# Kernel optimization log

Hardware: AMD Instinct MI355X
Metric: run time of the kernel (lower is better)

Reference implementation:

```python
import jax, jax.numpy as jnp
import numpy as np

N_NODES = 10000
N_EDGES = 320000
F_NODE = 16
NUM_BESSEL = 8
M = 32           # env_embed_multiplicity
LAT = 128        # latent dimension
R_MAX = 5.0
P_CUT = 6.0      # polynomial cutoff order
AVG_NEIGH = 32.0
SQRT3 = 1.7320508075688772
SQRT2 = 1.4142135623730951


def _mlp(x, weights):
    # nequip ScalarMLPFunction: linear layers with 1/sqrt(fan_in) norm, silu between layers
    h = x
    n = len(weights)
    for i, W in enumerate(weights):
        h = h @ W * (1.0 / np.sqrt(W.shape[0]))
        if i < n - 1:
            h = jax.nn.silu(h)
    return h


def _weight_channels(Y, w):
    # MakeWeightedChannels: Y [E,4] = (0e | 1e), w [E,M,2] per-irrep weights -> [E,M,4]
    return jnp.concatenate([w[..., 0:1] * Y[:, None, 0:1],
                            w[..., 1:2] * Y[:, None, 1:4]], axis=-1)


def setup_inputs():
    key = jax.random.key(0)
    ks = jax.random.split(key, 16)

    def w(k, i, o):
        return jax.random.normal(k, (i, o), jnp.float32)

    two_body_in = 2 * F_NODE + NUM_BESSEL  # 40
    return {
        "coordinates": jax.random.uniform(ks[0], (N_NODES, 3), jnp.float32),
        "node_attrs": jax.random.uniform(ks[1], (N_NODES, F_NODE), jnp.float32),
        "edge_index": jax.random.randint(ks[2], (2, N_EDGES), 0, N_NODES),
        "W2b0": w(ks[3], two_body_in, 64),
        "W2b1": w(ks[4], 64, 128),
        "W2b2": w(ks[5], 128, LAT),
        "Wenv0": w(ks[6], LAT, 4 * M),       # initial-edge embed + env weights (2 irreps each)
        "Wlat0": w(ks[7], LAT + 2 * M, 128),
        "Wlat1": w(ks[8], 128, LAT),
        "Ws0": w(ks[9], 2 * M, M),            # e3nn Linear, scalar block (2 paths)
        "Wv0": w(ks[10], 3 * M, M),           # e3nn Linear, vector block (3 paths)
        "Wenv1": w(ks[11], LAT, 2 * M),
        "Wfin0": w(ks[12], LAT + 2 * M, 128),
        "Wfin1": w(ks[13], 128, LAT),
    }


def reference(coordinates, node_attrs, edge_index, W2b0, W2b1, W2b2, Wenv0,
              Wlat0, Wlat1, Ws0, Wv0, Wenv1, Wfin0, Wfin1):
    sender, center = edge_index[0], edge_index[1]
    vec = coordinates[center] - coordinates[sender]            # [E,3]
    r = jnp.sqrt(jnp.sum(vec * vec, axis=-1) + 1e-12)          # [E]
    u = r / R_MAX
    p = P_CUT
    fcut = (1.0 - (p + 1.0) * (p + 2.0) / 2.0 * u**p
            + p * (p + 2.0) * u**(p + 1.0)
            - p * (p + 1.0) / 2.0 * u**(p + 2.0))
    fcut = jnp.where(u < 1.0, fcut, 0.0)
    n = jnp.arange(1, NUM_BESSEL + 1, dtype=jnp.float32)
    bessel = np.sqrt(2.0 / R_MAX) * jnp.sin(n * jnp.pi * u[:, None]) / r[:, None]
    edge_feats = bessel * fcut[:, None]                        # [E,8]
    unit = vec / r[:, None]
    Y = jnp.concatenate([jnp.ones_like(r)[:, None], SQRT3 * unit], axis=-1)  # [E,4] component-normalized SH

    inv_sqrt_n = 1.0 / np.sqrt(AVG_NEIGH)
    E = r.shape[0]

    # two-body latent (layer 0)
    lat_in = jnp.concatenate([node_attrs[center], node_attrs[sender], edge_feats], -1)
    lat = _mlp(lat_in, (W2b0, W2b1, W2b2)) * fcut[:, None]     # [E,LAT]
    w_all = lat @ Wenv0 * (1.0 / np.sqrt(LAT))                 # [E,4M]
    w_edge = w_all[:, :2 * M].reshape(E, M, 2)
    w_env = w_all[:, 2 * M:].reshape(E, M, 2)
    feat = _weight_channels(Y, w_edge)                         # [E,M,4] initial edge embed
    env = jax.ops.segment_sum(_weight_channels(Y, w_env), center, num_segments=N_NODES)
    env = env[center] * inv_sqrt_n                             # [E,M,4]

    fs, fv = feat[..., 0], feat[..., 1:]
    es, ev = env[..., 0], env[..., 1:]
    # layer-0 tensor product instruction list (uuu, no weights)
    p0 = fs * es                               # 0e x 0e -> 0e
    p1 = jnp.sum(fv * ev, -1) / SQRT3          # 1e x 1e -> 0e
    p2 = fs[..., None] * ev                    # 0e x 1e -> 1e
    p3 = fv * es[..., None]                    # 1e x 0e -> 1e
    p4 = jnp.cross(fv, ev) / SQRT2             # 1e x 1e -> 1e
    scal0 = jnp.concatenate([p0, p1], -1)      # [E,2M] scalar outs (n_scalar_outs=2)
    # per-layer e3nn Linear
    s_mix = scal0 @ Ws0 * (1.0 / np.sqrt(2 * M))                         # [E,M]
    v_mix = jnp.einsum('eic,io->eoc', jnp.concatenate([p2, p3, p4], 1), Wv0) * (1.0 / np.sqrt(3 * M))  # [E,M,3]

    # latent resnet update (update param 0 -> sigmoid = 0.5)
    alpha = 0.5
    c_old = 1.0 / np.sqrt(alpha * alpha + 1.0)
    c_new = alpha * c_old
    new_lat = _mlp(jnp.concatenate([lat, scal0], -1), (Wlat0, Wlat1)) * fcut[:, None]
    lat = c_old * lat + c_new * new_lat

    # layer 1 env embedding + tensor product (last layer -> scalars only)
    w_env1 = (lat @ Wenv1 * (1.0 / np.sqrt(LAT))).reshape(E, M, 2)
    env1 = jax.ops.segment_sum(_weight_channels(Y, w_env1), center, num_segments=N_NODES)
    env1 = env1[center] * inv_sqrt_n
    q0 = s_mix * env1[..., 0]
    q1 = jnp.sum(v_mix * env1[..., 1:], -1) / SQRT3
    scal1 = jnp.concatenate([q0, q1], -1)      # [E,2M]

    new_lat = _mlp(jnp.concatenate([lat, scal1], -1), (Wfin0, Wfin1)) * fcut[:, None]
    lat = c_old * lat + c_new * new_lat

    node_out = jax.ops.segment_sum(lat, center, num_segments=N_NODES) * inv_sqrt_n
    return node_out
```

## Files before the change

### kernel.cpp

```cpp
#include <hip/hip_runtime.h>
#include <hip/hip_bf16.h>
#include <math.h>

typedef __hip_bfloat16 bf16;
typedef unsigned short us;
typedef __attribute__((ext_vector_type(8))) short short8;
typedef __attribute__((ext_vector_type(4))) float floatx4;

#define INV_SQRT_N 0.17677669529663687f
#define INV_SQRT3  0.5773502691896258f
#define INV_SQRT2  0.7071067811865476f
#define C_OLD      0.8944271909999159f
#define C_NEW      0.4472135954999579f
#define PI_F       3.14159265358979323846f
#define SQRT3_F    1.7320508075688772f
#define BESSEL_PREF 0.6324555320336759f

__device__ __forceinline__ float b2f(bf16 x) { return __bfloat162float(x); }
__device__ __forceinline__ bf16  f2b(float x) { return __float2bfloat16(x); }
__device__ __forceinline__ us f2bu(float x) {
  bf16 h = f2b(x); us u; __builtin_memcpy(&u, &h, 2); return u;
}
__device__ __forceinline__ float silu_f(float v) { return v / (1.f + __expf(-v)); }
__device__ __forceinline__ floatx4 mfma16(short8 a, short8 b, floatx4 c) {
  return __builtin_amdgcn_mfma_f32_16x16x32_bf16(a, b, c, 0, 0, 0);
}
__device__ __forceinline__ short8 ld8(const void* p) {
  return *reinterpret_cast<const short8*>(p);
}
#define ZERO8 ((short8){0,0,0,0,0,0,0,0})

__global__ __launch_bounds__(256) void k_deg(
    const int* __restrict__ eidx, int E, int* __restrict__ deg) {
  int e = blockIdx.x * 256 + threadIdx.x;
  if (e < E) atomicAdd(&deg[eidx[E + e]], 1);
}

__global__ __launch_bounds__(1024) void k_scan(
    const int* __restrict__ deg, int N,
    int* __restrict__ rowptr, int* __restrict__ cursor) {
  __shared__ int part[1024];
  int t = threadIdx.x;
  int C = (N + 1023) / 1024;
  int base = t * C;
  int s = 0;
  for (int i = 0; i < C; ++i) { int idx = base + i; if (idx < N) s += deg[idx]; }
  part[t] = s;
  __syncthreads();
  for (int off = 1; off < 1024; off <<= 1) {
    int v = (t >= off) ? part[t - off] : 0;
    __syncthreads();
    part[t] += v;
    __syncthreads();
  }
  int excl = (t == 0) ? 0 : part[t - 1];
  for (int i = 0; i < C; ++i) {
    int idx = base + i;
    if (idx < N) { rowptr[idx] = excl; cursor[idx] = excl; excl += deg[idx]; }
  }
  if (t == 0) rowptr[N] = part[1023];
}

__global__ __launch_bounds__(256) void k_fill(
    const int* __restrict__ eidx, int E, int* __restrict__ cursor,
    int* __restrict__ eord, int* __restrict__ cent) {
  int e = blockIdx.x * 256 + threadIdx.x;
  if (e >= E) return;
  int c = eidx[E + e];
  int slot = atomicAdd(&cursor[c], 1);
  eord[slot] = e;
  cent[slot] = c;
}

__device__ __forceinline__ void wp(const float* W, us* Wt, int K, int NOUT, int t) {
  int n = t / K, k = t % K;
  Wt[n * K + k] = f2bu(W[k * NOUT + n]);
}

__global__ __launch_bounds__(256) void k_wprep_all(
    const float* W2b0, const float* W2b1, const float* W2b2,
    const float* Wenv0, const float* Wlat0, const float* Wlat1,
    const float* Wenv1, const float* Wfin0, const float* Wfin1,
    const float* Ws0, const float* Wv0,
    us* W2b0p, us* W2b1t, us* W2b2t, us* Wenv0t, us* Wlat0t, us* Wlat1t,
    us* Wenv1t, us* Wfin0t, us* Wfin1t, us* Wmixt) {
  int t = blockIdx.x * 256 + threadIdx.x;
  if (t < 8192)  { wp(W2b1,  W2b1t,  64, 128, t); return; } t -= 8192;
  if (t < 16384) { wp(W2b2,  W2b2t, 128, 128, t); return; } t -= 16384;
  if (t < 16384) { wp(Wenv0, Wenv0t,128, 128, t); return; } t -= 16384;
  if (t < 24576) { wp(Wlat0, Wlat0t,192, 128, t); return; } t -= 24576;
  if (t < 16384) { wp(Wlat1, Wlat1t,128, 128, t); return; } t -= 16384;
  if (t < 8192)  { wp(Wenv1, Wenv1t,128,  64, t); return; } t -= 8192;
  if (t < 24576) { wp(Wfin0, Wfin0t,192, 128, t); return; } t -= 24576;
  if (t < 16384) { wp(Wfin1, Wfin1t,128, 128, t); return; } t -= 16384;
  if (t < 4096)  {
    int n = t >> 6, k = t & 63;
    W2b0p[n * 64 + k] = (k < 40) ? f2bu(W2b0[k * 64 + n]) : 0;
    return;
  } t -= 4096;
  if (t < 5120) {
    int o = t / 160, k = t % 160;
    float v = (k < 64) ? Ws0[k * 32 + o] : Wv0[(k - 64) * 32 + o];
    Wmixt[o * 160 + k] = f2bu(v);
  }
}

__global__ __launch_bounds__(256) void k_envg(
    const bf16* __restrict__ wenv, const float* __restrict__ Yb,
    const int* __restrict__ rowptr, int N, float* __restrict__ env) {
  int t = blockIdx.x * 256 + threadIdx.x;
  if (t >= N * 32) return;
  int n = t >> 5, m = t & 31;
  int j0 = rowptr[n], j1 = rowptr[n + 1];
  float a0 = 0.f, a1 = 0.f, a2 = 0.f, a3 = 0.f;
  for (int j = j0; j < j1; ++j) {
    float w0 = b2f(wenv[(long)j*64 + 2*m]);
    float w1 = b2f(wenv[(long)j*64 + 2*m + 1]);
    float4 y = *reinterpret_cast<const float4*>(&Yb[(long)j*4]);
    a0 += w0;
    a1 += w1 * y.y;
    a2 += w1 * y.z;
    a3 += w1 * y.w;
  }
  *reinterpret_cast<float4*>(&env[(long)n*128 + m*4]) = make_float4(a0, a1, a2, a3);
}

__global__ __launch_bounds__(256) void k_nodeg(
    const bf16* __restrict__ lat, const int* __restrict__ rowptr,
    int N, float* __restrict__ out) {
  int t = blockIdx.x * 256 + threadIdx.x;
  if (t >= N * 128) return;
  int n = t >> 7, j = t & 127;
  int j0 = rowptr[n], j1 = rowptr[n + 1];
  float s = 0.f;
  for (int q = j0; q < j1; ++q)
    s += b2f(lat[(long)q*128 + j]);
  out[t] = s * INV_SQRT_N;
}

__global__ __launch_bounds__(256) void mfused3s(
    const float* __restrict__ coords, const float* __restrict__ nattr,
    const int* __restrict__ eidx, const int* __restrict__ eord,
    const us* __restrict__ W0p, const us* __restrict__ W1t,
    const us* __restrict__ W2t, const us* __restrict__ Wenv0t,
    bf16* __restrict__ lat, bf16* __restrict__ b64, bf16* __restrict__ wenv,
    float* __restrict__ fcut, float* __restrict__ Yb,
    float s40, float s64s, float s128, int E) {
  constexpr int AP = 72, HP = 136;
  __shared__ __align__(16) us SB[64 * 144];
  us* As = SB;
  us* H0 = SB + 64 * AP;
  us* Hs = SB;
  int tid = threadIdx.x;
  int lane = tid & 63, w = tid >> 6;
  int nl = lane & 15, quad = lane >> 4;
  long e0 = (long)blockIdx.x * 64;

  short8 w0f[2], w1f[2][2], w2f[4][2];
  #pragma unroll
  for (int kc = 0; kc < 2; ++kc)
    w0f[kc] = ld8(W0p + (w*16 + nl) * 64 + kc*32 + quad*8);
  #pragma unroll
  for (int kc = 0; kc < 2; ++kc)
    #pragma unroll
    for (int ct = 0; ct < 2; ++ct)
      w1f[kc][ct] = ld8(W1t + (long)(w*32 + ct*16 + nl) * 64 + kc*32 + quad*8);
  #pragma unroll
  for (int kc = 0; kc < 4; ++kc)
    #pragma unroll
    for (int ct = 0; ct < 2; ++ct)
      w2f[kc][ct] = ld8(W2t + (long)(w*32 + ct*16 + nl) * 128 + kc*32 + quad*8);

  {
    int row = tid & 63, q = tid >> 6;
    long eg = e0 + row;
    if (q == 3) {
      for (int i = 40; i < 64; ++i) As[row * AP + i] = 0;
    } else if (eg < E) {
      int e = eord[eg];
      int sN = eidx[e], cN = eidx[E + e];
      if (q == 0) {
        #pragma unroll
        for (int i = 0; i < 16; ++i)
          As[row * AP + i] = f2bu(nattr[(long)cN*16 + i]);
      } else if (q == 1) {
        #pragma unroll
        for (int i = 0; i < 16; ++i)
          As[row * AP + 16 + i] = f2bu(nattr[(long)sN*16 + i]);
      } else {
        float dx = coords[cN*3+0] - coords[sN*3+0];
        float dy = coords[cN*3+1] - coords[sN*3+1];
        float dz = coords[cN*3+2] - coords[sN*3+2];
        float r = sqrtf(dx*dx + dy*dy + dz*dz + 1e-12f);
        float u = r * 0.2f;
        float u3 = u*u*u;
        float u6 = u3*u3, u7 = u6*u, u8 = u7*u;
        float fc = 1.f - 28.f*u6 + 48.f*u7 - 21.f*u8;
        fc = (u < 1.f) ? fc : 0.f;
        float inv_r = 1.f / r;
        fcut[eg] = fc;
        Yb[eg*4+0] = 1.f;
        Yb[eg*4+1] = SQRT3_F * dx * inv_r;
        Yb[eg*4+2] = SQRT3_F * dy * inv_r;
        Yb[eg*4+3] = SQRT3_F * dz * inv_r;
        float pref = BESSEL_PREF * inv_r * fc;
        #pragma unroll
        for (int n = 1; n <= 8; ++n)
          As[row * AP + 32 + n - 1] = f2bu(pref * sinf((float)n * PI_F * u));
      }
    } else {
      if (q == 0) {
        for (int i = 0; i < 16; ++i) As[row * AP + i] = 0;
      } else if (q == 1) {
        for (int i = 0; i < 16; ++i) As[row * AP + 16 + i] = 0;
      } else {
        for (int i = 32; i < 40; ++i) As[row * AP + i] = 0;
      }
    }
  }
  __syncthreads();

  floatx4 a0[4];
  #pragma unroll
  for (int i = 0; i < 4; ++i) a0[i] = (floatx4){0.f,0.f,0.f,0.f};
  #pragma unroll
  for (int kc = 0; kc < 2; ++kc) {
    short8 af[4];
    #pragma unroll
    for (int et = 0; et < 4; ++et)
      af[et] = ld8(&As[(et*16 + nl) * AP + kc*32 + quad*8]);
    #pragma unroll
    for (int et = 0; et < 4; ++et) a0[et] = mfma16(af[et], w0f[kc], a0[et]);
  }
  #pragma unroll
  for (int et = 0; et < 4; ++et)
    #pragma unroll
    for (int r = 0; r < 4; ++r)
      H0[(et*16 + quad*4 + r) * AP + w*16 + nl] = f2bu(silu_f(a0[et][r] * s40));
  __syncthreads();

  floatx4 acc[4][2];
  #pragma unroll
  for (int i = 0; i < 4; ++i)
    #pragma unroll
    for (int j = 0; j < 2; ++j) acc[i][j] = (floatx4){0.f,0.f,0.f,0.f};
  #pragma unroll
  for (int kc = 0; kc < 2; ++kc) {
    short8 af[4];
    #pragma unroll
    for (int et = 0; et < 4; ++et)
      af[et] = ld8(&H0[(et*16 + nl) * AP + kc*32 + quad*8]);
    #pragma unroll
    for (int et = 0; et < 4; ++et)
      #pragma unroll
      for (int ct = 0; ct < 2; ++ct)
        acc[et][ct] = mfma16(af[et], w1f[kc][ct], acc[et][ct]);
  }
  __syncthreads();

  #pragma unroll
  for (int et = 0; et < 4; ++et)
    #pragma unroll
    for (int ct = 0; ct < 2; ++ct)
      #pragma unroll
      for (int r = 0; r < 4; ++r)
        Hs[(et*16 + quad*4 + r) * HP + w*32 + ct*16 + nl] =
            f2bu(silu_f(acc[et][ct][r] * s64s));
  __syncthreads();

  #pragma unroll
  for (int i = 0; i < 4; ++i)
    #pragma unroll
    for (int j = 0; j < 2; ++j) acc[i][j] = (floatx4){0.f,0.f,0.f,0.f};
  #pragma unroll
  for (int kc = 0; kc < 4; ++kc) {
    short8 af[4];
    #pragma unroll
    for (int et = 0; et < 4; ++et)
      af[et] = ld8(&Hs[(et*16 + nl) * HP + kc*32 + quad*8]);
    #pragma unroll
    for (int et = 0; et < 4; ++et)
      #pragma unroll
      for (int ct = 0; ct < 2; ++ct)
        acc[et][ct] = mfma16(af[et], w2f[kc][ct], acc[et][ct]);
  }

  short8 wef[4][2];
  #pragma unroll
  for (int kc = 0; kc < 4; ++kc)
    #pragma unroll
    for (int ct = 0; ct < 2; ++ct)
      wef[kc][ct] = ld8(Wenv0t + (long)(w*32 + ct*16 + nl) * 128 + kc*32 + quad*8);

  __syncthreads();

  #pragma unroll
  for (int et = 0; et < 4; ++et)
    #pragma unroll
    for (int ct = 0; ct < 2; ++ct)
      #pragma unroll
      for (int r = 0; r < 4; ++r) {
        long eg = e0 + et*16 + quad*4 + r;
        int col = w*32 + ct*16 + nl;
        us lv = 0;
        if (eg < E) {
          lv = f2bu(acc[et][ct][r] * s128 * fcut[eg]);
          bf16 h; __builtin_memcpy(&h, &lv, 2);
          lat[eg * 128 + col] = h;
        }
        Hs[(et*16 + quad*4 + r) * HP + col] = lv;
      }
  __syncthreads();

  #pragma unroll
  for (int i = 0; i < 4; ++i)
    #pragma unroll
    for (int j = 0; j < 2; ++j) acc[i][j] = (floatx4){0.f,0.f,0.f,0.f};
  #pragma unroll
  for (int kc = 0; kc < 4; ++kc) {
    short8 af[4];
    #pragma unroll
    for (int et = 0; et < 4; ++et)
      af[et] = ld8(&Hs[(et*16 + nl) * HP + kc*32 + quad*8]);
    #pragma unroll
    for (int et = 0; et < 4; ++et)
      #pragma unroll
      for (int ct = 0; ct < 2; ++ct)
        acc[et][ct] = mfma16(af[et], wef[kc][ct], acc[et][ct]);
  }
  #pragma unroll
  for (int et = 0; et < 4; ++et)
    #pragma unroll
    for (int ct = 0; ct < 2; ++ct)
      #pragma unroll
      for (int r = 0; r < 4; ++r) {
        long eg = e0 + et*16 + quad*4 + r;
        if (eg >= E) continue;
        int col = w*32 + ct*16 + nl;
        float v = acc[et][ct][r] * s128;
        if (col < 64) b64[eg * 64 + col] = f2b(v);
        else          wenv[eg * 64 + (col - 64)] = f2b(v);
      }
}

__global__ __launch_bounds__(256) void mf_lat(
    const bf16* __restrict__ A, const bf16* __restrict__ wedge,
    const float* __restrict__ env, const float* __restrict__ Yb,
    const int* __restrict__ cent,
    const us* __restrict__ W0t, const us* __restrict__ W1t,
    const us* __restrict__ Wenv1t,
    bf16* __restrict__ outb, bf16* __restrict__ wenv1,
    const float* __restrict__ fcut,
    float scale0, float scale1, int E) {
  constexpr int K = 192, KP = 200, NC0 = 6, HP = 136;
  __shared__ __align__(16) us SB[64 * KP];
  us* As = SB;
  us* Hs = SB;
  int tid = threadIdx.x;
  int lane = tid & 63, w = tid >> 6;
  int nl = lane & 15, quad = lane >> 4;
  long e0 = (long)blockIdx.x * 64;
  int m = tid & 31;

  #pragma unroll
  for (int it = 0; it < 8; ++it) {
    int el = (tid >> 5) + it * 8;
    long e = e0 + el;
    us v0 = 0, v1 = 0;
    if (e < E) {
      int c = cent[e];
      float w0 = b2f(wedge[e*64 + 2*m]), w1 = b2f(wedge[e*64 + 2*m + 1]);
      float4 ev = *(const float4*)(env + (long)c*128 + m*4);
      float4 y  = *(const float4*)(Yb + e*4);
      float es  = ev.x * INV_SQRT_N;
      float evx = ev.y * INV_SQRT_N, evy = ev.z * INV_SQRT_N, evz = ev.w * INV_SQRT_N;
      float fvx = w1*y.y, fvy = w1*y.z, fvz = w1*y.w;
      v0 = f2bu(w0 * es);
      v1 = f2bu((fvx*evx + fvy*evy + fvz*evz) * INV_SQRT3);
    }
    As[el * KP + 128 + m] = v0;
    As[el * KP + 160 + m] = v1;
  }

  #pragma unroll
  for (int it = 0; it < 4; ++it) {
    int i = tid + it * 256;
    int row = i >> 4, col = (i & 15) * 8;
    long eg = e0 + row;
    short8 v = (eg < E) ? ld8(A + eg * 128 + col) : ZERO8;
    *(short8*)&As[row * KP + col] = v;
  }

  short8 w0f[NC0][2];
  #pragma unroll
  for (int kc = 0; kc < NC0; ++kc)
    #pragma unroll
    for (int ct = 0; ct < 2; ++ct)
      w0f[kc][ct] = ld8(W0t + (long)(w*32 + ct*16 + nl) * K + kc*32 + quad*8);
  __syncthreads();

  floatx4 acc[4][2];
  #pragma unroll
  for (int i = 0; i < 4; ++i)
    #pragma unroll
    for (int j = 0; j < 2; ++j) acc[i][j] = (floatx4){0.f,0.f,0.f,0.f};
  #pragma unroll
  for (int kc = 0; kc < NC0; ++kc) {
    short8 af[4];
    #pragma unroll
    for (int et = 0; et < 4; ++et)
      af[et] = ld8(&As[(et*16 + nl) * KP + kc*32 + quad*8]);
    #pragma unroll
    for (int et = 0; et < 4; ++et)
      #pragma unroll
      for (int ct = 0; ct < 2; ++ct)
        acc[et][ct] = mfma16(af[et], w0f[kc][ct], acc[et][ct]);
  }

  short8 w1f[4][2];
  #pragma unroll
  for (int kc = 0; kc < 4; ++kc)
    #pragma unroll
    for (int ct = 0; ct < 2; ++ct)
      w1f[kc][ct] = ld8(W1t + (long)(w*32 + ct*16 + nl) * 128 + kc*32 + quad*8);

  __syncthreads();

  #pragma unroll
  for (int et = 0; et < 4; ++et)
    #pragma unroll
    for (int ct = 0; ct < 2; ++ct)
      #pragma unroll
      for (int r = 0; r < 4; ++r)
        Hs[(et*16 + quad*4 + r) * HP + w*32 + ct*16 + nl] =
            f2bu(silu_f(acc[et][ct][r] * scale0));
  __syncthreads();

  #pragma unroll
  for (int i = 0; i < 4; ++i)
    #pragma unroll
    for (int j = 0; j < 2; ++j) acc[i][j] = (floatx4){0.f,0.f,0.f,0.f};
  #pragma unroll
  for (int kc = 0; kc < 4; ++kc) {
    short8 af[4];
    #pragma unroll
    for (int et = 0; et < 4; ++et)
      af[et] = ld8(&Hs[(et*16 + nl) * HP + kc*32 + quad*8]);
    #pragma unroll
    for (int et = 0; et < 4; ++et)
      #pragma unroll
      for (int ct = 0; ct < 2; ++ct)
        acc[et][ct] = mfma16(af[et], w1f[kc][ct], acc[et][ct]);
  }

  short8 wef[4];
  #pragma unroll
  for (int kc = 0; kc < 4; ++kc)
    wef[kc] = ld8(Wenv1t + (long)(w*16 + nl) * 128 + kc*32 + quad*8);

  __syncthreads();

  #pragma unroll
  for (int et = 0; et < 4; ++et)
    #pragma unroll
    for (int ct = 0; ct < 2; ++ct)
      #pragma unroll
      for (int r = 0; r < 4; ++r) {
        long eg = e0 + et*16 + quad*4 + r;
        int col = w*32 + ct*16 + nl;
        us lv = 0;
        if (eg < E) {
          float v = acc[et][ct][r] * scale1 * fcut[eg];
          long idx = eg * 128 + col;
          lv = f2bu(C_OLD * b2f(outb[idx]) + C_NEW * v);
          bf16 h; __builtin_memcpy(&h, &lv, 2);
          outb[idx] = h;
        }
        Hs[(et*16 + quad*4 + r) * HP + col] = lv;
      }
  __syncthreads();

  floatx4 acc2[4];
  #pragma unroll
  for (int i = 0; i < 4; ++i) acc2[i] = (floatx4){0.f,0.f,0.f,0.f};
  #pragma unroll
  for (int kc = 0; kc < 4; ++kc) {
    short8 af[4];
    #pragma unroll
    for (int et = 0; et < 4; ++et)
      af[et] = ld8(&Hs[(et*16 + nl) * HP + kc*32 + quad*8]);
    #pragma unroll
    for (int et = 0; et < 4; ++et)
      acc2[et] = mfma16(af[et], wef[kc], acc2[et]);
  }
  #pragma unroll
  for (int et = 0; et < 4; ++et)
    #pragma unroll
    for (int r = 0; r < 4; ++r) {
      long eg = e0 + et*16 + quad*4 + r;
      if (eg >= E) continue;
      wenv1[eg * 64 + w*16 + nl] = f2b(acc2[et][r] * 0.08838834764831845f);
    }
}

__global__ __launch_bounds__(256) void mf_fin(
    const bf16* __restrict__ A, const bf16* __restrict__ wedge,
    const float* __restrict__ env, const float* __restrict__ env1,
    const float* __restrict__ Yb, const int* __restrict__ cent,
    const us* __restrict__ Wm,
    const us* __restrict__ W0t, const us* __restrict__ W1t,
    bf16* __restrict__ outb, const float* __restrict__ fcut,
    float scale0, float scale1, int E) {
  constexpr int K = 192, KP = 200, HP = 136, PP = 360, RP = 132, NC0 = 6;
  __shared__ __align__(16) us SB[64 * PP];
  __shared__ __align__(16) us Wl[32 * 160];
  us* P = SB;
  float* R = (float*)SB;
  us* As = SB;
  us* Hs = SB;
  int tid = threadIdx.x;
  int lane = tid & 63, w = tid >> 6;
  int nl = lane & 15, quad = lane >> 4;
  long e0 = (long)blockIdx.x * 64;
  int m = tid & 31;

  for (int i = tid; i < 640; i += 256)
    *(short8*)&Wl[i * 8] = ld8(Wm + i * 8);

  #pragma unroll
  for (int it = 0; it < 8; ++it) {
    int el = (tid >> 5) + it * 8;
    long e = e0 + el;
    if (e < E) {
      int c = cent[e];
      float w0 = b2f(wedge[e*64 + 2*m]), w1 = b2f(wedge[e*64 + 2*m + 1]);
      float4 ev4 = *(const float4*)(env + (long)c*128 + m*4);
      float4 y   = *(const float4*)(Yb + e*4);
      float es  = ev4.x * INV_SQRT_N;
      float evx = ev4.y * INV_SQRT_N, evy = ev4.z * INV_SQRT_N, evz = ev4.w * INV_SQRT_N;
      float fvx = w1*y.y, fvy = w1*y.z, fvz = w1*y.w;
      us* p = P + el * PP;
      p[m]       = f2bu(w0 * es);
      p[32 + m]  = f2bu((fvx*evx + fvy*evy + fvz*evz) * INV_SQRT3);
      p[64 + m]  = f2bu(w0 * evx);
      p[96 + m]  = f2bu(fvx * es);
      p[128 + m] = f2bu((fvy*evz - fvz*evy) * INV_SQRT2);
      p[160 + m] = f2bu(w0 * evy);
      p[192 + m] = f2bu(fvy * es);
      p[224 + m] = f2bu((fvz*evx - fvx*evz) * INV_SQRT2);
      p[256 + m] = f2bu(w0 * evz);
      p[288 + m] = f2bu(fvz * es);
      p[320 + m] = f2bu((fvx*evy - fvy*evx) * INV_SQRT2);
    } else {
      us* p = P + el * PP;
      #pragma unroll
      for (int q = 0; q < 11; ++q) p[q*32 + m] = 0;
    }
  }
  __syncthreads();

  floatx4 acc[4][2];
  #pragma unroll
  for (int i = 0; i < 4; ++i)
    #pragma unroll
    for (int j = 0; j < 2; ++j) acc[i][j] = (floatx4){0.f,0.f,0.f,0.f};
  {
    int pbase  = (w == 0) ? 0 : 64 + (w - 1) * 96;
    int wkbase = (w == 0) ? 0 : 64;
    int ksteps = (w == 0) ? 2 : 3;
    for (int ks = 0; ks < ksteps; ++ks) {
      short8 af[4], bv[2];
      #pragma unroll
      for (int et = 0; et < 4; ++et)
        af[et] = ld8(&P[(et*16 + nl) * PP + pbase + ks*32 + quad*8]);
      #pragma unroll
      for (int ct = 0; ct < 2; ++ct)
        bv[ct] = ld8(&Wl[(ct*16 + nl) * 160 + wkbase + ks*32 + quad*8]);
      #pragma unroll
      for (int et = 0; et < 4; ++et)
        #pragma unroll
        for (int ct = 0; ct < 2; ++ct)
          acc[et][ct] = mfma16(af[et], bv[ct], acc[et][ct]);
    }
  }
  __syncthreads();

  #pragma unroll
  for (int et = 0; et < 4; ++et)
    #pragma unroll
    for (int ct = 0; ct < 2; ++ct)
      #pragma unroll
      for (int r = 0; r < 4; ++r) {
        int el = et*16 + quad*4 + r;
        R[el * RP + w*32 + ct*16 + nl] = acc[et][ct][r];
      }
  __syncthreads();

  float qa[8], qb[8];
  #pragma unroll
  for (int it = 0; it < 8; ++it) {
    int el = (tid >> 5) + it * 8;
    long e = e0 + el;
    qa[it] = 0.f; qb[it] = 0.f;
    if (e < E) {
      int c = cent[e];
      float4 e1 = *(const float4*)(env1 + (long)c*128 + m*4);
      float sr = R[el * RP + m];
      float vx = R[el * RP + 32 + m];
      float vy = R[el * RP + 64 + m];
      float vz = R[el * RP + 96 + m];
      qa[it] = sr * 0.125f * (e1.x * INV_SQRT_N);
      qb[it] = (vx*e1.y + vy*e1.z + vz*e1.w) *
               (0.10206207261596577f * INV_SQRT_N * INV_SQRT3);
    }
  }
  __syncthreads();

  #pragma unroll
  for (int it = 0; it < 4; ++it) {
    int i = tid + it * 256;
    int row = i >> 4, col = (i & 15) * 8;
    long eg = e0 + row;
    short8 v = (eg < E) ? ld8(A + eg * 128 + col) : ZERO8;
    *(short8*)&As[row * KP + col] = v;
  }
  #pragma unroll
  for (int it = 0; it < 8; ++it) {
    int el = (tid >> 5) + it * 8;
    As[el * KP + 128 + m] = f2bu(qa[it]);
    As[el * KP + 160 + m] = f2bu(qb[it]);
  }

  short8 w0f[NC0][2];
  #pragma unroll
  for (int kc = 0; kc < NC0; ++kc)
    #pragma unroll
    for (int ct = 0; ct < 2; ++ct)
      w0f[kc][ct] = ld8(W0t + (long)(w*32 + ct*16 + nl) * K + kc*32 + quad*8);
  __syncthreads();

  #pragma unroll
  for (int i = 0; i < 4; ++i)
    #pragma unroll
    for (int j = 0; j < 2; ++j) acc[i][j] = (floatx4){0.f,0.f,0.f,0.f};
  #pragma unroll
  for (int kc = 0; kc < NC0; ++kc) {
    short8 af[4];
    #pragma unroll
    for (int et = 0; et < 4; ++et)
      af[et] = ld8(&As[(et*16 + nl) * KP + kc*32 + quad*8]);
    #pragma unroll
    for (int et = 0; et < 4; ++et)
      #pragma unroll
      for (int ct = 0; ct < 2; ++ct)
        acc[et][ct] = mfma16(af[et], w0f[kc][ct], acc[et][ct]);
  }

  short8 w1f[4][2];
  #pragma unroll
  for (int kc = 0; kc < 4; ++kc)
    #pragma unroll
    for (int ct = 0; ct < 2; ++ct)
      w1f[kc][ct] = ld8(W1t + (long)(w*32 + ct*16 + nl) * 128 + kc*32 + quad*8);

  __syncthreads();

  #pragma unroll
  for (int et = 0; et < 4; ++et)
    #pragma unroll
    for (int ct = 0; ct < 2; ++ct)
      #pragma unroll
      for (int r = 0; r < 4; ++r)
        Hs[(et*16 + quad*4 + r) * HP + w*32 + ct*16 + nl] =
            f2bu(silu_f(acc[et][ct][r] * scale0));
  __syncthreads();

  #pragma unroll
  for (int i = 0; i < 4; ++i)
    #pragma unroll
    for (int j = 0; j < 2; ++j) acc[i][j] = (floatx4){0.f,0.f,0.f,0.f};
  #pragma unroll
  for (int kc = 0; kc < 4; ++kc) {
    short8 af[4];
    #pragma unroll
    for (int et = 0; et < 4; ++et)
      af[et] = ld8(&Hs[(et*16 + nl) * HP + kc*32 + quad*8]);
    #pragma unroll
    for (int et = 0; et < 4; ++et)
      #pragma unroll
      for (int ct = 0; ct < 2; ++ct)
        acc[et][ct] = mfma16(af[et], w1f[kc][ct], acc[et][ct]);
  }

  #pragma unroll
  for (int et = 0; et < 4; ++et)
    #pragma unroll
    for (int ct = 0; ct < 2; ++ct)
      #pragma unroll
      for (int r = 0; r < 4; ++r) {
        long eg = e0 + et*16 + quad*4 + r;
        if (eg >= E) continue;
        int col = w*32 + ct*16 + nl;
        float v = acc[et][ct][r] * scale1 * fcut[eg];
        long idx = eg * 128 + col;
        outb[idx] = f2b(C_OLD * b2f(outb[idx]) + C_NEW * v);
      }
}

extern "C" void kernel_launch(void* const* d_in, const int* in_sizes, int n_in,
                              void* d_out, int out_size, void* d_ws, size_t ws_size,
                              hipStream_t stream) {
  const float* coords = (const float*)d_in[0];
  const float* nattr  = (const float*)d_in[1];
  const int*   eidx   = (const int*)d_in[2];
  const float* W2b0   = (const float*)d_in[3];
  const float* W2b1   = (const float*)d_in[4];
  const float* W2b2   = (const float*)d_in[5];
  const float* Wenv0  = (const float*)d_in[6];
  const float* Wlat0  = (const float*)d_in[7];
  const float* Wlat1  = (const float*)d_in[8];
  const float* Ws0    = (const float*)d_in[9];
  const float* Wv0    = (const float*)d_in[10];
  const float* Wenv1  = (const float*)d_in[11];
  const float* Wfin0  = (const float*)d_in[12];
  const float* Wfin1  = (const float*)d_in[13];
  float* out = (float*)d_out;
  int E = in_sizes[2] / 2;
  int N = in_sizes[0] / 3;

  float* fcut   = (float*)d_ws;
  float* Yb     = fcut + (size_t)E;
  float* env    = Yb + (size_t)E*4;
  float* env1   = env + (size_t)N*128;
  int*   deg    = (int*)(env1 + (size_t)N*128);
  int*   rowptr = deg + N;
  int*   cursor = rowptr + (N + 8);
  int*   eord   = cursor + N;
  int*   cent   = eord + E;
  bf16*  b64    = (bf16*)(cent + E);
  bf16*  lat    = b64 + (size_t)E*64;
  bf16*  S      = lat + (size_t)E*128;
  us* W2b1t  = (us*)(S + (size_t)E*64);
  us* W2b2t  = W2b1t + 128*64;
  us* Wenv0t = W2b2t + 128*128;
  us* Wlat0t = Wenv0t + 128*128;
  us* Wlat1t = Wlat0t + 128*192;
  us* Wenv1t = Wlat1t + 128*128;
  us* Wfin0t = Wenv1t + 64*128;
  us* Wfin1t = Wfin0t + 128*192;
  us* W2b0p  = Wfin1t + 128*128;
  us* Wmixt  = W2b0p + 64*64;

  hipMemsetAsync(deg, 0, (size_t)N * sizeof(int), stream);

  dim3 blk(256);
  const float s40  = 0.15811388300841897f;
  const float s64  = 0.125f;
  const float s128 = 0.08838834764831845f;
  const float s192 = 0.07216878364870323f;
  int gB = (E + 63) / 64;
  int gE = (E + 255) / 256;

  k_deg<<<gE, blk, 0, stream>>>(eidx, E, deg);
  k_scan<<<1, 1024, 0, stream>>>(deg, N, rowptr, cursor);
  k_fill<<<gE, blk, 0, stream>>>(eidx, E, cursor, eord, cent);
  k_wprep_all<<<dim3(548), blk, 0, stream>>>(
      W2b0, W2b1, W2b2, Wenv0, Wlat0, Wlat1, Wenv1, Wfin0, Wfin1, Ws0, Wv0,
      W2b0p, W2b1t, W2b2t, Wenv0t, Wlat0t, Wlat1t, Wenv1t, Wfin0t, Wfin1t, Wmixt);

  mfused3s<<<gB, blk, 0, stream>>>(
      coords, nattr, eidx, eord, W2b0p, W2b1t, W2b2t, Wenv0t,
      lat, b64, S , fcut, Yb, s40, s64, s128, E);

  k_envg<<<dim3((N*32 + 255) / 256), blk, 0, stream>>>(
      S , Yb, rowptr, N, env);

  mf_lat<<<gB, blk, 0, stream>>>(
      lat, b64, env, Yb, cent, Wlat0t, Wlat1t, Wenv1t,
      lat, S , fcut, s192, s128, E);

  k_envg<<<dim3((N*32 + 255) / 256), blk, 0, stream>>>(
      S , Yb, rowptr, N, env1);

  mf_fin<<<gB, blk, 0, stream>>>(
      lat, b64, env, env1, Yb, cent, Wmixt, Wfin0t, Wfin1t,
      lat, fcut, s192, s128, E);

  k_nodeg<<<dim3((N*128 + 255) / 256), blk, 0, stream>>>(
      lat, rowptr, N, out);
}
```

Before: 713.0 us.

## Halve LDS footprint in mf_fin by processing edges in two halves

The mixing stage of mf_fin now processes 64 edges as two halves of 32, so the shared buffer shrinks to the size needed for the later GEMM staging. The mixing weights are loaded directly into registers instead of being staged in shared memory. This cuts per-block LDS substantially to allow more resident blocks per CU. In exchange it adds extra barriers and holds more register fragments, which could raise register pressure.

```diff
diff --git a/kernel.cpp b/kernel.cpp
--- a/kernel.cpp
+++ b/kernel.cpp
@@ -512,8 +512,7 @@
     bf16* __restrict__ outb, const float* __restrict__ fcut,
     float scale0, float scale1, int E) {
   constexpr int K = 192, KP = 200, HP = 136, PP = 360, RP = 132, NC0 = 6;
-  __shared__ __align__(16) us SB[64 * PP];
-  __shared__ __align__(16) us Wl[32 * 160];
+  __shared__ __align__(16) us SB[64 * KP];
   us* P = SB;
   float* R = (float*)SB;
   us* As = SB;
@@ -524,97 +523,102 @@
   long e0 = (long)blockIdx.x * 64;
   int m = tid & 31;
 
-  for (int i = tid; i < 640; i += 256)
-    *(short8*)&Wl[i * 8] = ld8(Wm + i * 8);
-
-  #pragma unroll
-  for (int it = 0; it < 8; ++it) {
-    int el = (tid >> 5) + it * 8;
-    long e = e0 + el;
-    if (e < E) {
-      int c = cent[e];
-      float w0 = b2f(wedge[e*64 + 2*m]), w1 = b2f(wedge[e*64 + 2*m + 1]);
-      float4 ev4 = *(const float4*)(env + (long)c*128 + m*4);
-      float4 y   = *(const float4*)(Yb + e*4);
-      float es  = ev4.x * INV_SQRT_N;
-      float evx = ev4.y * INV_SQRT_N, evy = ev4.z * INV_SQRT_N, evz = ev4.w * INV_SQRT_N;
-      float fvx = w1*y.y, fvy = w1*y.z, fvz = w1*y.w;
-      us* p = P + el * PP;
-      p[m]       = f2bu(w0 * es);
-      p[32 + m]  = f2bu((fvx*evx + fvy*evy + fvz*evz) * INV_SQRT3);
-      p[64 + m]  = f2bu(w0 * evx);
-      p[96 + m]  = f2bu(fvx * es);
-      p[128 + m] = f2bu((fvy*evz - fvz*evy) * INV_SQRT2);
-      p[160 + m] = f2bu(w0 * evy);
-      p[192 + m] = f2bu(fvy * es);
-      p[224 + m] = f2bu((fvz*evx - fvx*evz) * INV_SQRT2);
-      p[256 + m] = f2bu(w0 * evz);
-      p[288 + m] = f2bu(fvz * es);
-      p[320 + m] = f2bu((fvx*evy - fvy*evx) * INV_SQRT2);
-    } else {
-      us* p = P + el * PP;
-      #pragma unroll
-      for (int q = 0; q < 11; ++q) p[q*32 + m] = 0;
+  int pbase  = (w == 0) ? 0 : 64 + (w - 1) * 96;
+  int wkbase = (w == 0) ? 0 : 64;
+  int ksteps = (w == 0) ? 2 : 3;
+  short8 wmf[3][2];
+  #pragma unroll
+  for (int ks = 0; ks < 3; ++ks)
+    #pragma unroll
+    for (int ct = 0; ct < 2; ++ct)
+      wmf[ks][ct] = (ks < ksteps)
+          ? ld8(Wm + (long)(ct*16 + nl) * 160 + wkbase + ks*32 + quad*8)
+          : ZERO8;
+
+  float qa[8], qb[8];
+  for (int half = 0; half < 2; ++half) {
+    long eh = e0 + half * 32;
+    #pragma unroll
+    for (int it = 0; it < 4; ++it) {
+      int el = (tid >> 5) + it * 8;
+      long e = eh + el;
+      if (e < E) {
+        int c = cent[e];
+        float w0 = b2f(wedge[e*64 + 2*m]), w1 = b2f(wedge[e*64 + 2*m + 1]);
+        float4 ev4 = *(const float4*)(env + (long)c*128 + m*4);
+        float4 y   = *(const float4*)(Yb + e*4);
+        float es  = ev4.x * INV_SQRT_N;
+        float evx = ev4.y * INV_SQRT_N, evy = ev4.z * INV_SQRT_N, evz = ev4.w * INV_SQRT_N;
+        float fvx = w1*y.y, fvy = w1*y.z, fvz = w1*y.w;
+        us* p = P + el * PP;
+        p[m]       = f2bu(w0 * es);
+        p[32 + m]  = f2bu((fvx*evx + fvy*evy + fvz*evz) * INV_SQRT3);
+        p[64 + m]  = f2bu(w0 * evx);
+        p[96 + m]  = f2bu(fvx * es);
+        p[128 + m] = f2bu((fvy*evz - fvz*evy) * INV_SQRT2);
+        p[160 + m] = f2bu(w0 * evy);
+        p[192 + m] = f2bu(fvy * es);
+        p[224 + m] = f2bu((fvz*evx - fvx*evz) * INV_SQRT2);
+        p[256 + m] = f2bu(w0 * evz);
+        p[288 + m] = f2bu(fvz * es);
+        p[320 + m] = f2bu((fvx*evy - fvy*evx) * INV_SQRT2);
+      } else {
+        us* p = P + el * PP;
+        #pragma unroll
+        for (int q = 0; q < 11; ++q) p[q*32 + m] = 0;
+      }
     }
-  }
-  __syncthreads();
-
-  floatx4 acc[4][2];
-  #pragma unroll
-  for (int i = 0; i < 4; ++i)
-    #pragma unroll
-    for (int j = 0; j < 2; ++j) acc[i][j] = (floatx4){0.f,0.f,0.f,0.f};
-  {
-    int pbase  = (w == 0) ? 0 : 64 + (w - 1) * 96;
-    int wkbase = (w == 0) ? 0 : 64;
-    int ksteps = (w == 0) ? 2 : 3;
+    __syncthreads();
+
+    floatx4 macc[2][2];
+    #pragma unroll
+    for (int i = 0; i < 2; ++i)
+      #pragma unroll
+      for (int j = 0; j < 2; ++j) macc[i][j] = (floatx4){0.f,0.f,0.f,0.f};
     for (int ks = 0; ks < ksteps; ++ks) {
-      short8 af[4], bv[2];
-      #pragma unroll
-      for (int et = 0; et < 4; ++et)
+      short8 af[2];
+      #pragma unroll
+      for (int et = 0; et < 2; ++et)
         af[et] = ld8(&P[(et*16 + nl) * PP + pbase + ks*32 + quad*8]);
       #pragma unroll
-      for (int ct = 0; ct < 2; ++ct)
-        bv[ct] = ld8(&Wl[(ct*16 + nl) * 160 + wkbase + ks*32 + quad*8]);
-      #pragma unroll
-      for (int et = 0; et < 4; ++et)
+      for (int et = 0; et < 2; ++et)
         #pragma unroll
         for (int ct = 0; ct < 2; ++ct)
-          acc[et][ct] = mfma16(af[et], bv[ct], acc[et][ct]);
+          macc[et][ct] = mfma16(af[et], wmf[ks][ct], macc[et][ct]);
     }
-  }
-  __syncthreads();
-
-  #pragma unroll
-  for (int et = 0; et < 4; ++et)
-    #pragma unroll
-    for (int ct = 0; ct < 2; ++ct)
-      #pragma unroll
-      for (int r = 0; r < 4; ++r) {
-        int el = et*16 + quad*4 + r;
-        R[el * RP + w*32 + ct*16 + nl] = acc[et][ct][r];
+    __syncthreads();
+
+    #pragma unroll
+    for (int et = 0; et < 2; ++et)
+      #pragma unroll
+      for (int ct = 0; ct < 2; ++ct)
+        #pragma unroll
+        for (int r = 0; r < 4; ++r) {
+          int el = et*16 + quad*4 + r;
+          R[el * RP + w*32 + ct*16 + nl] = macc[et][ct][r];
+        }
+    __syncthreads();
+
+    #pragma unroll
+    for (int it = 0; it < 4; ++it) {
+      int el = (tid >> 5) + it * 8;
+      long e = eh + el;
+      int qi = half*4 + it;
+      qa[qi] = 0.f; qb[qi] = 0.f;
+      if (e < E) {
+        int c = cent[e];
+        float4 e1 = *(const float4*)(env1 + (long)c*128 + m*4);
+        float sr = R[el * RP + m];
+        float vx = R[el * RP + 32 + m];
+        float vy = R[el * RP + 64 + m];
+        float vz = R[el * RP + 96 + m];
+        qa[qi] = sr * 0.125f * (e1.x * INV_SQRT_N);
+        qb[qi] = (vx*e1.y + vy*e1.z + vz*e1.w) *
+                 (0.10206207261596577f * INV_SQRT_N * INV_SQRT3);
       }
-  __syncthreads();
-
-  float qa[8], qb[8];
-  #pragma unroll
-  for (int it = 0; it < 8; ++it) {
-    int el = (tid >> 5) + it * 8;
-    long e = e0 + el;
-    qa[it] = 0.f; qb[it] = 0.f;
-    if (e < E) {
-      int c = cent[e];
-      float4 e1 = *(const float4*)(env1 + (long)c*128 + m*4);
-      float sr = R[el * RP + m];
-      float vx = R[el * RP + 32 + m];
-      float vy = R[el * RP + 64 + m];
-      float vz = R[el * RP + 96 + m];
-      qa[it] = sr * 0.125f * (e1.x * INV_SQRT_N);
-      qb[it] = (vx*e1.y + vy*e1.z + vz*e1.w) *
-               (0.10206207261596577f * INV_SQRT_N * INV_SQRT3);
     }
-  }
-  __syncthreads();
+    __syncthreads();
+  }
 
   #pragma unroll
   for (int it = 0; it < 4; ++it) {
@@ -625,11 +629,14 @@
     *(short8*)&As[row * KP + col] = v;
   }
   #pragma unroll
-  for (int it = 0; it < 8; ++it) {
-    int el = (tid >> 5) + it * 8;
-    As[el * KP + 128 + m] = f2bu(qa[it]);
-    As[el * KP + 160 + m] = f2bu(qb[it]);
-  }
+  for (int half = 0; half < 2; ++half)
+    #pragma unroll
+    for (int it = 0; it < 4; ++it) {
+      int el = half*32 + (tid >> 5) + it * 8;
+      int qi = half*4 + it;
+      As[el * KP + 128 + m] = f2bu(qa[qi]);
+      As[el * KP + 160 + m] = f2bu(qb[qi]);
+    }
 
   short8 w0f[NC0][2];
   #pragma unroll
@@ -639,6 +646,7 @@
       w0f[kc][ct] = ld8(W0t + (long)(w*32 + ct*16 + nl) * K + kc*32 + quad*8);
   __syncthreads();
 
+  floatx4 acc[4][2];
   #pragma unroll
   for (int i = 0; i < 4; ++i)
     #pragma unroll
```

Measured after the change: 893.8 us. 25.4% more time.
